# Kernel tuning notes

Hardware: AMD Instinct MI355X
Metric: run time of the kernel (lower is better)

The kernel has to match this reference:

```python
import jax, jax.numpy as jnp
import numpy as np

B, N, HIST, D, E, NH = 1024, 2, 64, 256, 128, 8
HD = D // NH


def _linear_params(key, fan_in, fan_out):
    kw, kb = jax.random.split(key)
    lim = 1.0 / np.sqrt(fan_in)
    W = jax.random.uniform(kw, (fan_in, fan_out), jnp.float32, -lim, lim)
    b = jax.random.uniform(kb, (fan_out,), jnp.float32, -lim, lim)
    return W, b


def setup_inputs() -> dict:
    key = jax.random.key(0)
    ks = jax.random.split(key, 11)
    inp = {
        "node_features": jax.random.normal(ks[0], (B, N, HIST, D), jnp.float32),
        "edge_features": jax.random.normal(ks[1], (B, E), jnp.float32),
    }
    inp["Wq"], inp["bq"] = _linear_params(ks[2], D, D)
    inp["Wk"], inp["bk"] = _linear_params(ks[3], D, D)
    inp["Wv"], inp["bv"] = _linear_params(ks[4], D, D)
    inp["Wo"], inp["bo"] = _linear_params(ks[5], D, D)
    inp["Wbias"], inp["bbias"] = _linear_params(ks[6], E, NH)
    inp["Wgate"], inp["bgate"] = _linear_params(ks[7], E, D)
    inp["Wscale"], inp["bscale"] = _linear_params(ks[8], E, D)
    inp["Wshift"], inp["bshift"] = _linear_params(ks[9], E, D)
    inp["Whead"], inp["bhead"] = _linear_params(ks[10], E, NH)
    return inp


def reference(node_features, edge_features, Wq, bq, Wk, bk, Wv, bv, Wo, bo,
              Wbias, bbias, Wgate, bgate, Wscale, bscale, Wshift, bshift,
              Whead, bhead) -> jnp.ndarray:
    b, n, hist, d = node_features.shape
    s = n * hist  # seq_len (temporal mode)
    x = node_features.reshape(b, s, d)

    Q = x @ Wq + bq
    K = x @ Wk + bk
    V = x @ Wv + bv

    # Edge-conditioned modulation of V (ECC-style gate/scale/shift)
    gate = jax.nn.sigmoid(edge_features @ Wgate + bgate)      # [b, d]
    scale = jnp.tanh(edge_features @ Wscale + bscale)         # [b, d]
    shift = edge_features @ Wshift + bshift                   # [b, d]
    V = (V * (1.0 + scale[:, None, :]) + shift[:, None, :]) * gate[:, None, :]

    # [b, nh, s, hd]
    Q = Q.reshape(b, s, NH, HD).transpose(0, 2, 1, 3)
    K = K.reshape(b, s, NH, HD).transpose(0, 2, 1, 3)
    V = V.reshape(b, s, NH, HD).transpose(0, 2, 1, 3)

    scores = jnp.einsum('bhqd,bhkd->bhqk', Q, K) * (1.0 / np.sqrt(HD))

    edge_bias = edge_features @ Wbias + bbias                 # [b, nh]
    head_scale = jnp.tanh(edge_features @ Whead + bhead)      # [b, nh]
    scores = scores * (1.0 + head_scale[:, :, None, None])

    # attention bias: edge_bias placed at (t, hist+t) and (hist+t, t)
    t = jnp.arange(hist)
    eb = jnp.broadcast_to(edge_bias[:, :, None], (b, NH, hist))
    attention_bias = jnp.zeros((b, NH, s, s), scores.dtype)
    attention_bias = attention_bias.at[:, :, t, hist + t].set(eb)
    attention_bias = attention_bias.at[:, :, hist + t, t].set(eb)

    attn = jax.nn.softmax(scores + attention_bias, axis=-1)   # dropout in eval mode = identity
    out = jnp.einsum('bhqk,bhkd->bhqd', attn, V)
    out = out.transpose(0, 2, 1, 3).reshape(b, n, hist, d)
    out = out[:, :, -1, :]                                    # last timestep per node
    return out @ Wo + bo
```

## Files before the change

### kernel.cpp

```cpp
#include <hip/hip_runtime.h>
#include <cstdint>
#include <cstddef>


typedef short bf16x8 __attribute__((ext_vector_type(8)));
typedef float f32x4 __attribute__((ext_vector_type(4)));

#define MFMA16(A, B, C) __builtin_amdgcn_mfma_f32_16x16x32_bf16((A), (B), (C), 0, 0, 0)

static __device__ __forceinline__ uint16_t f2bf(float f) {
    uint32_t u = __builtin_bit_cast(uint32_t, f);
    u += 0x7FFFu + ((u >> 16) & 1u);
    return (uint16_t)(u >> 16);
}
static __device__ __forceinline__ uint32_t pack2(float a, float b) {
    return (uint32_t)f2bf(a) | ((uint32_t)f2bf(b) << 16);
}

__global__ __launch_bounds__(256) void k_prep(
    const float* __restrict__ Wq, const float* __restrict__ Wv,
    const float* __restrict__ Wo, const float* __restrict__ Wk,
    uint16_t* __restrict__ WqT, uint16_t* __restrict__ WvT,
    uint16_t* __restrict__ WoT, uint16_t* __restrict__ WkB,
    const float* __restrict__ edge,
    const float* __restrict__ Wgate, const float* __restrict__ bgate,
    const float* __restrict__ Wscale, const float* __restrict__ bscale,
    const float* __restrict__ Wshift, const float* __restrict__ bshift,
    const float* __restrict__ Wbias, const float* __restrict__ bbias,
    const float* __restrict__ Whead, const float* __restrict__ bhead,
    float* __restrict__ sp, float* __restrict__ tp, float* __restrict__ ebhs)
{
    __shared__ float smem[64 * 65];
    const int t = threadIdx.x;
    const int bid = blockIdx.x;
    if (bid < 64) {
        const int z = bid >> 4, tr = (bid >> 2) & 3, tc = bid & 3;
        if (z == 3) {
            #pragma unroll
            for (int i = 0; i < 16; i++) {
                int flat = i * 256 + t;
                int lr = flat >> 6, lc = flat & 63;
                WkB[(size_t)(tr * 64 + lr) * 264 + tc * 64 + lc] =
                    f2bf(Wk[(size_t)(tr * 64 + lr) * 256 + tc * 64 + lc]);
            }
            return;
        }
        const float* W = (z == 0) ? Wq : ((z == 1) ? Wv : Wo);
        uint16_t* O = (z == 0) ? WqT : ((z == 1) ? WvT : WoT);
        float (*tile)[65] = (float (*)[65])smem;
        #pragma unroll
        for (int i = 0; i < 16; i++) {
            int flat = i * 256 + t;
            int lr = flat >> 6, lc = flat & 63;
            tile[lr][lc] = W[(size_t)(tr * 64 + lr) * 256 + tc * 64 + lc];
        }
        __syncthreads();
        #pragma unroll
        for (int i = 0; i < 16; i++) {
            int flat = i * 256 + t;
            int orow = flat >> 6, oc = flat & 63;
            O[(size_t)(tc * 64 + orow) * 264 + tr * 64 + oc] = f2bf(tile[oc][orow]);
        }
        return;
    }
    float* eL = smem;
    const int b0 = (bid - 64) * 4;
    for (int idx = t; idx < 512; idx += 256) {
        int bi = idx >> 7, e = idx & 127;
        eL[bi * 128 + e] = edge[(size_t)(b0 + bi) * 128 + e];
    }
    __syncthreads();
    float ag[4] = {0, 0, 0, 0}, asr[4] = {0, 0, 0, 0}, ah[4] = {0, 0, 0, 0};
    for (int e = 0; e < 128; e++) {
        float wg = Wgate[e * 256 + t];
        float wsc = Wscale[e * 256 + t];
        float wsh = Wshift[e * 256 + t];
        #pragma unroll
        for (int bi = 0; bi < 4; bi++) {
            float xv = eL[bi * 128 + e];
            ag[bi] = fmaf(xv, wg, ag[bi]);
            asr[bi] = fmaf(xv, wsc, asr[bi]);
            ah[bi] = fmaf(xv, wsh, ah[bi]);
        }
    }
    float bg = bgate[t], bs = bscale[t], bsh = bshift[t];
    #pragma unroll
    for (int bi = 0; bi < 4; bi++) {
        float g = 1.0f / (1.0f + __expf(-(ag[bi] + bg)));
        float sc = tanhf(asr[bi] + bs);
        float sh = ah[bi] + bsh;
        sp[(size_t)(b0 + bi) * 256 + t] = (1.0f + sc) * g;
        tp[(size_t)(b0 + bi) * 256 + t] = sh * g;
    }
    if (t < 64) {
        int bi = t >> 4, o = t & 15, h = o & 7;
        const float* W = (o < 8) ? Wbias : Whead;
        float a = 0.0f;
        for (int e = 0; e < 128; e++) a = fmaf(eL[bi * 128 + e], W[e * 8 + h], a);
        float val = (o < 8) ? (a + bbias[h]) : tanhf(a + bhead[h]);
        ebhs[(size_t)(b0 + bi) * 16 + o] = val;
    }
}

__global__ __launch_bounds__(256) void k_qu(
    const float* __restrict__ node, const uint16_t* __restrict__ WqT,
    const uint16_t* __restrict__ WkB, const float* __restrict__ bq,
    uint16_t* __restrict__ U)
{
    __shared__ uint16_t xq[16 * 264];
    __shared__ uint16_t QL[16 * 264];
    const int t = threadIdx.x, lane = t & 63, w = t >> 6, c = lane & 15, quad = lane >> 4;
    const int b0 = blockIdx.x * 4;
    #pragma unroll
    for (int i = 0; i < 4; i++) {
        int flat4 = i * 256 + t;
        int row = flat4 >> 6, c4 = flat4 & 63;
        int r = row & 7;
        int bb = b0 + (r >> 1);
        int s = (r & 1) ? 127 : 63;
        const float4 v = *(const float4*)(node + ((size_t)(bb * 128 + s)) * 256 + c4 * 4);
        uint2 pv; pv.x = pack2(v.x, v.y); pv.y = pack2(v.z, v.w);
        *(uint2*)&xq[row * 264 + c4 * 4] = pv;
    }
    __syncthreads();
    f32x4 zero = {0, 0, 0, 0};
    f32x4 acc[4];
    #pragma unroll
    for (int i = 0; i < 4; i++) acc[i] = zero;
    #pragma unroll
    for (int kk = 0; kk < 8; kk++) {
        bf16x8 afr = *(const bf16x8*)&xq[c * 264 + kk * 32 + quad * 8];
        #pragma unroll
        for (int i = 0; i < 4; i++) {
            int nt = w * 4 + i;
            bf16x8 bfr = *(const bf16x8*)&WqT[(size_t)(nt * 16 + c) * 264 + kk * 32 + quad * 8];
            acc[i] = MFMA16(afr, bfr, acc[i]);
        }
    }
    #pragma unroll
    for (int i = 0; i < 4; i++) {
        int nt = w * 4 + i;
        float bqv = bq[nt * 16 + c];
        #pragma unroll
        for (int r = 0; r < 4; r++) {
            QL[(quad * 4 + r) * 264 + nt * 16 + c] = f2bf(acc[i][r] + bqv);
        }
    }
    __syncthreads();
    for (int hh = 0; hh < 8; hh++) {
        bf16x8 bfr = *(const bf16x8*)&QL[c * 264 + hh * 32 + quad * 8];
        #pragma unroll
        for (int i = 0; i < 4; i++) {
            int mt = w * 4 + i;
            bf16x8 afr = *(const bf16x8*)&WkB[(size_t)(mt * 16 + c) * 264 + hh * 32 + quad * 8];
            f32x4 d = MFMA16(afr, bfr, zero);
            if (c < 8) {
                int bb = b0 + (c >> 1);
                int qh = (c & 1) * 8 + hh;
                uint2 pk; pk.x = pack2(d[0], d[1]); pk.y = pack2(d[2], d[3]);
                *(uint2*)&U[((size_t)(bb * 16 + qh)) * 256 + mt * 16 + quad * 4] = pk;
            }
        }
    }
}

__global__ __launch_bounds__(256, 3) void k_main(
    const float* __restrict__ node,
    const uint16_t* __restrict__ U,
    const float* __restrict__ ebhs,
    uint16_t* __restrict__ Y)
{
    __shared__ uint16_t xc[64 * 264];
    __shared__ uint16_t uL[16 * 264];
    __shared__ uint16_t pL[16 * 72];
    __shared__ float wred[2][16][4];
    __shared__ float stM[16], stL[16], stA[16];
    __shared__ float ebhsL[16];
    const int b = blockIdx.x;
    const int t = threadIdx.x, lane = t & 63, w = t >> 6, c = lane & 15, quad = lane >> 4;
    #pragma unroll
    for (int i = 0; i < 2; i++) {
        int flat = i * 256 + t;
        int row = flat >> 5, c16 = flat & 31;
        uint4 v = *(const uint4*)&U[((size_t)b * 16 + row) * 256 + c16 * 8];
        *(uint4*)&uL[row * 264 + c16 * 8] = v;
    }
    if (t < 16) { ebhsL[t] = ebhs[(size_t)b * 16 + t]; stM[t] = -1e30f; stL[t] = 0.0f; }
    __syncthreads();
    const int q = c >> 3, h = c & 7;
    const float scaleF = 0.17677669529663687f * (1.0f + ebhsL[8 + h]);
    const float ebv = ebhsL[h];
    f32x4 zero = {0, 0, 0, 0};
    f32x4 yacc[4];
    #pragma unroll
    for (int tt = 0; tt < 4; tt++) yacc[tt] = zero;

    for (int ch = 0; ch < 2; ch++) {
        #pragma unroll
        for (int i = 0; i < 16; i++) {
            int flat4 = i * 256 + t;
            int row = flat4 >> 6, c4 = flat4 & 63;
            const float4 v = *(const float4*)(node + ((size_t)b * 128 + ch * 64 + row) * 256 + c4 * 4);
            uint2 pv; pv.x = pack2(v.x, v.y); pv.y = pack2(v.z, v.w);
            int col = (c4 * 4 + ((row >> 3) & 3) * 16) & 255;
            *(uint2*)&xc[row * 264 + col] = pv;
        }
        __syncthreads();
        f32x4 sacc = zero;
        {
            int arow = w * 16 + c;
            int sh = ((arow >> 3) & 3) * 16;
            #pragma unroll
            for (int kk = 0; kk < 8; kk++) {
                int colA = (kk * 32 + quad * 8 + sh) & 255;
                bf16x8 afr = *(const bf16x8*)&xc[arow * 264 + colA];
                bf16x8 bfr = *(const bf16x8*)&uL[c * 264 + kk * 32 + quad * 8];
                sacc = MFMA16(afr, bfr, sacc);
            }
        }
        float v0[4];
        #pragma unroll
        for (int r = 0; r < 4; r++) {
            int krow = ch * 64 + w * 16 + quad * 4 + r;
            float x = sacc[r] * scaleF;
            if ((q == 0 && krow == 127) || (q == 1 && krow == 63)) x += ebv;
            v0[r] = x;
        }
        float lmax = fmaxf(fmaxf(v0[0], v0[1]), fmaxf(v0[2], v0[3]));
        lmax = fmaxf(lmax, __shfl_xor(lmax, 16, 64));
        lmax = fmaxf(lmax, __shfl_xor(lmax, 32, 64));
        if (lane < 16) wred[0][c][w] = lmax;
        __syncthreads();
        float cmax = fmaxf(fmaxf(wred[0][c][0], wred[0][c][1]), fmaxf(wred[0][c][2], wred[0][c][3]));
        float mold = stM[c];
        float mnew = fmaxf(mold, cmax);
        float alpha = __expf(mold - mnew);
        float p0[4]; float lsum = 0.0f;
        #pragma unroll
        for (int r = 0; r < 4; r++) { p0[r] = __expf(v0[r] - mnew); lsum += p0[r]; }
        lsum += __shfl_xor(lsum, 16, 64);
        lsum += __shfl_xor(lsum, 32, 64);
        if (lane < 16) wred[1][c][w] = lsum;
        __syncthreads();
        if (w == 0 && lane < 16) {
            float csum = wred[1][c][0] + wred[1][c][1] + wred[1][c][2] + wred[1][c][3];
            stL[c] = stL[c] * alpha + csum;
            stM[c] = mnew;
            stA[c] = alpha;
        }
        {
            uint2 pk; pk.x = pack2(p0[0], p0[1]); pk.y = pack2(p0[2], p0[3]);
            *(uint2*)&pL[c * 72 + w * 16 + quad * 4] = pk;
        }
        __syncthreads();
        float av[4];
        #pragma unroll
        for (int r = 0; r < 4; r++) av[r] = stA[quad * 4 + r];
        #pragma unroll
        for (int tt = 0; tt < 4; tt++)
            #pragma unroll
            for (int r = 0; r < 4; r++) yacc[tt][r] *= av[r];
        #pragma unroll
        for (int kk = 0; kk < 2; kk++) {
            bf16x8 afr = *(const bf16x8*)&pL[c * 72 + kk * 32 + quad * 8];
            int kbase = kk * 32 + quad * 8;
            int sh = ((kbase >> 3) & 3) * 16;
            #pragma unroll
            for (int tt = 0; tt < 4; tt++) {
                int n = w * 64 + tt * 16 + c;
                int col = (n + sh) & 255;
                union { bf16x8 v; uint32_t u[4]; } bb;
                #pragma unroll
                for (int jj = 0; jj < 4; jj++) {
                    uint32_t lo = xc[(kbase + 2 * jj) * 264 + col];
                    uint32_t hi = xc[(kbase + 2 * jj + 1) * 264 + col];
                    bb.u[jj] = lo | (hi << 16);
                }
                yacc[tt] = MFMA16(afr, bb.v, yacc[tt]);
            }
        }
        __syncthreads();
    }
    float invl[4];
    #pragma unroll
    for (int r = 0; r < 4; r++) invl[r] = 1.0f / stL[quad * 4 + r];
    #pragma unroll
    for (int tt = 0; tt < 4; tt++) {
        int n = w * 64 + tt * 16 + c;
        #pragma unroll
        for (int r = 0; r < 4; r++) {
            int qh = quad * 4 + r;
            int hq = qh & 7, qq = qh >> 3;
            Y[((size_t)(hq * 2048 + b * 2 + qq)) * 256 + n] = f2bf(yacc[tt][r] * invl[r]);
        }
    }
}

__global__ __launch_bounds__(256) void k_out(
    const uint16_t* __restrict__ Y,
    const uint16_t* __restrict__ WvT, const uint16_t* __restrict__ WoT,
    const float* __restrict__ bv, const float* __restrict__ bo,
    const float* __restrict__ sp, const float* __restrict__ tp,
    float* __restrict__ out)
{
    __shared__ uint16_t yh[2 * 16 * 264];
    __shared__ uint16_t zm[16 * 264];
    const int t = threadIdx.x, lane = t & 63, w = t >> 6, c = lane & 15, quad = lane >> 4;
    const int R0 = blockIdx.x * 16;
    f32x4 zero = {0, 0, 0, 0};
    for (int hp = 0; hp < 4; hp++) {
        __syncthreads();
        #pragma unroll
        for (int i = 0; i < 4; i++) {
            int flat = i * 256 + t;
            int hl = flat >> 9, rem = flat & 511;
            int row = rem >> 5, c16 = rem & 31;
            uint4 v = *(const uint4*)&Y[((size_t)((2 * hp + hl) * 2048 + R0 + row)) * 256 + c16 * 8];
            *(uint4*)&yh[(hl * 16 + row) * 264 + c16 * 8] = v;
        }
        __syncthreads();
        int hl = w >> 1, nt = w & 1;
        int h = 2 * hp + hl;
        f32x4 zacc = zero;
        #pragma unroll
        for (int kk = 0; kk < 8; kk++) {
            bf16x8 afr = *(const bf16x8*)&yh[(hl * 16 + c) * 264 + kk * 32 + quad * 8];
            bf16x8 bfr = *(const bf16x8*)&WvT[(size_t)(h * 32 + nt * 16 + c) * 264 + kk * 32 + quad * 8];
            zacc = MFMA16(afr, bfr, zacc);
        }
        int col = h * 32 + nt * 16 + c;
        float bvv = bv[col];
        #pragma unroll
        for (int r = 0; r < 4; r++) {
            int row = quad * 4 + r;
            int b = (R0 + row) >> 1;
            float z = zacc[r] + bvv;
            zm[row * 264 + col] = f2bf(z * sp[(size_t)b * 256 + col] + tp[(size_t)b * 256 + col]);
        }
    }
    __syncthreads();
    #pragma unroll
    for (int i = 0; i < 4; i++) {
        int nt = w * 4 + i;
        int n = nt * 16 + c;
        f32x4 fa = zero;
        #pragma unroll
        for (int kk = 0; kk < 8; kk++) {
            bf16x8 afr = *(const bf16x8*)&zm[c * 264 + kk * 32 + quad * 8];
            bf16x8 bfr = *(const bf16x8*)&WoT[(size_t)n * 264 + kk * 32 + quad * 8];
            fa = MFMA16(afr, bfr, fa);
        }
        float bov = bo[n];
        #pragma unroll
        for (int r = 0; r < 4; r++) {
            out[(size_t)(R0 + quad * 4 + r) * 256 + n] = fa[r] + bov;
        }
    }
}

extern "C" void kernel_launch(void* const* d_in, const int* in_sizes, int n_in,
                              void* d_out, int out_size, void* d_ws, size_t ws_size,
                              hipStream_t stream) {
    const float* node   = (const float*)d_in[0];
    const float* edge   = (const float*)d_in[1];
    const float* Wq     = (const float*)d_in[2];
    const float* bq     = (const float*)d_in[3];
    const float* Wk     = (const float*)d_in[4];
    const float* Wv     = (const float*)d_in[6];
    const float* bv     = (const float*)d_in[7];
    const float* Wo     = (const float*)d_in[8];
    const float* bo     = (const float*)d_in[9];
    const float* Wbias  = (const float*)d_in[10];
    const float* bbias  = (const float*)d_in[11];
    const float* Wgate  = (const float*)d_in[12];
    const float* bgate  = (const float*)d_in[13];
    const float* Wscale = (const float*)d_in[14];
    const float* bscale = (const float*)d_in[15];
    const float* Wshift = (const float*)d_in[16];
    const float* bshift = (const float*)d_in[17];
    const float* Whead  = (const float*)d_in[18];
    const float* bhead  = (const float*)d_in[19];

    char* ws = (char*)d_ws;
    uint16_t* WqT  = (uint16_t*)(ws + 0);
    uint16_t* WvT  = (uint16_t*)(ws + 135168);
    uint16_t* WoT  = (uint16_t*)(ws + 270336);
    uint16_t* WkB  = (uint16_t*)(ws + 405504);
    float*    spw  = (float*)(ws + 540672);
    float*    tpw  = (float*)(ws + 1589248);
    float*    ebhs = (float*)(ws + 2637824);
    uint16_t* Uw   = (uint16_t*)(ws + 2703360);
    uint16_t* Yw   = (uint16_t*)(ws + 11091968);

    k_prep<<<320, 256, 0, stream>>>(Wq, Wv, Wo, Wk, WqT, WvT, WoT, WkB,
                                    edge, Wgate, bgate, Wscale, bscale, Wshift, bshift,
                                    Wbias, bbias, Whead, bhead, spw, tpw, ebhs);
    k_qu<<<256, 256, 0, stream>>>(node, WqT, WkB, bq, Uw);
    k_main<<<1024, 256, 0, stream>>>(node, Uw, ebhs, Yw);
    k_out<<<128, 256, 0, stream>>>(Yw, WvT, WoT, bv, bo, spw, tpw, (float*)d_out);
}
```

Baseline: 286.7 us.

## Compute full score rows per wave and prefetch second chunk into registers

```diff
diff --git a/kernel.cpp b/kernel.cpp
--- a/kernel.cpp
+++ b/kernel.cpp
@@ -172,12 +172,11 @@
 {
     __shared__ uint16_t xc[64 * 264];
     __shared__ uint16_t uL[16 * 264];
-    __shared__ uint16_t pL[16 * 72];
-    __shared__ float wred[2][16][4];
-    __shared__ float stM[16], stL[16], stA[16];
+    __shared__ uint16_t pL[4 * 16 * 72];
     __shared__ float ebhsL[16];
     const int b = blockIdx.x;
     const int t = threadIdx.x, lane = t & 63, w = t >> 6, c = lane & 15, quad = lane >> 4;
+
     #pragma unroll
     for (int i = 0; i < 2; i++) {
         int flat = i * 256 + t;
@@ -185,8 +184,25 @@
         uint4 v = *(const uint4*)&U[((size_t)b * 16 + row) * 256 + c16 * 8];
         *(uint4*)&uL[row * 264 + c16 * 8] = v;
     }
-    if (t < 16) { ebhsL[t] = ebhs[(size_t)b * 16 + t]; stM[t] = -1e30f; stL[t] = 0.0f; }
+    if (t < 16) ebhsL[t] = ebhs[(size_t)b * 16 + t];
+
+    float4 R[16];
+    #pragma unroll
+    for (int i = 0; i < 16; i++) {
+        int flat4 = i * 256 + t;
+        int row = flat4 >> 6, c4 = flat4 & 63;
+        R[i] = *(const float4*)(node + ((size_t)b * 128 + row) * 256 + c4 * 4);
+    }
+    #pragma unroll
+    for (int i = 0; i < 16; i++) {
+        int flat4 = i * 256 + t;
+        int row = flat4 >> 6, c4 = flat4 & 63;
+        uint2 pv; pv.x = pack2(R[i].x, R[i].y); pv.y = pack2(R[i].z, R[i].w);
+        int col = (c4 * 4 + ((row >> 3) & 3) * 16) & 255;
+        *(uint2*)&xc[row * 264 + col] = pv;
+    }
     __syncthreads();
+
     const int q = c >> 3, h = c & 7;
     const float scaleF = 0.17677669529663687f * (1.0f + ebhsL[8 + h]);
     const float ebv = ebhsL[h];
@@ -194,75 +210,76 @@
     f32x4 yacc[4];
     #pragma unroll
     for (int tt = 0; tt < 4; tt++) yacc[tt] = zero;
-
+    float mrow = -1e30f, lrow = 0.0f;
+    uint16_t* pW = &pL[w * 16 * 72];
+
+    #pragma unroll
     for (int ch = 0; ch < 2; ch++) {
-        #pragma unroll
-        for (int i = 0; i < 16; i++) {
-            int flat4 = i * 256 + t;
-            int row = flat4 >> 6, c4 = flat4 & 63;
-            const float4 v = *(const float4*)(node + ((size_t)b * 128 + ch * 64 + row) * 256 + c4 * 4);
-            uint2 pv; pv.x = pack2(v.x, v.y); pv.y = pack2(v.z, v.w);
-            int col = (c4 * 4 + ((row >> 3) & 3) * 16) & 255;
-            *(uint2*)&xc[row * 264 + col] = pv;
-        }
-        __syncthreads();
-        f32x4 sacc = zero;
-        {
-            int arow = w * 16 + c;
-            int sh = ((arow >> 3) & 3) * 16;
-            #pragma unroll
-            for (int kk = 0; kk < 8; kk++) {
+        if (ch == 0) {
+            #pragma unroll
+            for (int i = 0; i < 16; i++) {
+                int flat4 = i * 256 + t;
+                int row = flat4 >> 6, c4 = flat4 & 63;
+                R[i] = *(const float4*)(node + ((size_t)b * 128 + 64 + row) * 256 + c4 * 4);
+            }
+        }
+        f32x4 sacc[4];
+        #pragma unroll
+        for (int kt = 0; kt < 4; kt++) sacc[kt] = zero;
+        #pragma unroll
+        for (int kk = 0; kk < 8; kk++) {
+            bf16x8 bfr = *(const bf16x8*)&uL[c * 264 + kk * 32 + quad * 8];
+            #pragma unroll
+            for (int kt = 0; kt < 4; kt++) {
+                int arow = kt * 16 + c;
+                int sh = ((arow >> 3) & 3) * 16;
                 int colA = (kk * 32 + quad * 8 + sh) & 255;
                 bf16x8 afr = *(const bf16x8*)&xc[arow * 264 + colA];
-                bf16x8 bfr = *(const bf16x8*)&uL[c * 264 + kk * 32 + quad * 8];
-                sacc = MFMA16(afr, bfr, sacc);
-            }
-        }
-        float v0[4];
-        #pragma unroll
-        for (int r = 0; r < 4; r++) {
-            int krow = ch * 64 + w * 16 + quad * 4 + r;
-            float x = sacc[r] * scaleF;
-            if ((q == 0 && krow == 127) || (q == 1 && krow == 63)) x += ebv;
-            v0[r] = x;
-        }
-        float lmax = fmaxf(fmaxf(v0[0], v0[1]), fmaxf(v0[2], v0[3]));
+                sacc[kt] = MFMA16(afr, bfr, sacc[kt]);
+            }
+        }
+        float v0[4][4];
+        float lmax = -1e30f;
+        #pragma unroll
+        for (int kt = 0; kt < 4; kt++) {
+            #pragma unroll
+            for (int r = 0; r < 4; r++) {
+                int krow = ch * 64 + kt * 16 + quad * 4 + r;
+                float x = sacc[kt][r] * scaleF;
+                if ((q == 0 && krow == 127) || (q == 1 && krow == 63)) x += ebv;
+                v0[kt][r] = x;
+                lmax = fmaxf(lmax, x);
+            }
+        }
         lmax = fmaxf(lmax, __shfl_xor(lmax, 16, 64));
         lmax = fmaxf(lmax, __shfl_xor(lmax, 32, 64));
-        if (lane < 16) wred[0][c][w] = lmax;
-        __syncthreads();
-        float cmax = fmaxf(fmaxf(wred[0][c][0], wred[0][c][1]), fmaxf(wred[0][c][2], wred[0][c][3]));
-        float mold = stM[c];
-        float mnew = fmaxf(mold, cmax);
-        float alpha = __expf(mold - mnew);
-        float p0[4]; float lsum = 0.0f;
-        #pragma unroll
-        for (int r = 0; r < 4; r++) { p0[r] = __expf(v0[r] - mnew); lsum += p0[r]; }
+        float mnew = fmaxf(mrow, lmax);
+        float alpha = __expf(mrow - mnew);
+        float lsum = 0.0f;
+        #pragma unroll
+        for (int kt = 0; kt < 4; kt++) {
+            uint2 pk;
+            float p0 = __expf(v0[kt][0] - mnew);
+            float p1 = __expf(v0[kt][1] - mnew);
+            float p2 = __expf(v0[kt][2] - mnew);
+            float p3 = __expf(v0[kt][3] - mnew);
+            lsum += (p0 + p1) + (p2 + p3);
+            pk.x = pack2(p0, p1); pk.y = pack2(p2, p3);
+            *(uint2*)&pW[c * 72 + kt * 16 + quad * 4] = pk;
+        }
         lsum += __shfl_xor(lsum, 16, 64);
         lsum += __shfl_xor(lsum, 32, 64);
-        if (lane < 16) wred[1][c][w] = lsum;
-        __syncthreads();
-        if (w == 0 && lane < 16) {
-            float csum = wred[1][c][0] + wred[1][c][1] + wred[1][c][2] + wred[1][c][3];
-            stL[c] = stL[c] * alpha + csum;
-            stM[c] = mnew;
-            stA[c] = alpha;
-        }
-        {
-            uint2 pk; pk.x = pack2(p0[0], p0[1]); pk.y = pack2(p0[2], p0[3]);
-            *(uint2*)&pL[c * 72 + w * 16 + quad * 4] = pk;
-        }
-        __syncthreads();
-        float av[4];
-        #pragma unroll
-        for (int r = 0; r < 4; r++) av[r] = stA[quad * 4 + r];
-        #pragma unroll
-        for (int tt = 0; tt < 4; tt++)
-            #pragma unroll
-            for (int r = 0; r < 4; r++) yacc[tt][r] *= av[r];
+        lrow = lrow * alpha + lsum;
+        mrow = mnew;
+        #pragma unroll
+        for (int r = 0; r < 4; r++) {
+            float aj = __shfl(alpha, quad * 4 + r, 64);
+            #pragma unroll
+            for (int tt = 0; tt < 4; tt++) yacc[tt][r] *= aj;
+        }
         #pragma unroll
         for (int kk = 0; kk < 2; kk++) {
-            bf16x8 afr = *(const bf16x8*)&pL[c * 72 + kk * 32 + quad * 8];
+            bf16x8 afr = *(const bf16x8*)&pW[c * 72 + kk * 32 + quad * 8];
             int kbase = kk * 32 + quad * 8;
             int sh = ((kbase >> 3) & 3) * 16;
             #pragma unroll
@@ -279,19 +296,29 @@
                 yacc[tt] = MFMA16(afr, bb.v, yacc[tt]);
             }
         }
-        __syncthreads();
-    }
-    float invl[4];
-    #pragma unroll
-    for (int r = 0; r < 4; r++) invl[r] = 1.0f / stL[quad * 4 + r];
-    #pragma unroll
-    for (int tt = 0; tt < 4; tt++) {
-        int n = w * 64 + tt * 16 + c;
-        #pragma unroll
-        for (int r = 0; r < 4; r++) {
+        if (ch == 0) {
+            __syncthreads();
+            #pragma unroll
+            for (int i = 0; i < 16; i++) {
+                int flat4 = i * 256 + t;
+                int row = flat4 >> 6, c4 = flat4 & 63;
+                uint2 pv; pv.x = pack2(R[i].x, R[i].y); pv.y = pack2(R[i].z, R[i].w);
+                int col = (c4 * 4 + ((row >> 3) & 3) * 16) & 255;
+                *(uint2*)&xc[row * 264 + col] = pv;
+            }
+            __syncthreads();
+        }
+    }
+    float invr = 1.0f / lrow;
+    #pragma unroll
+    for (int r = 0; r < 4; r++) {
+        float invj = __shfl(invr, quad * 4 + r, 64);
+        #pragma unroll
+        for (int tt = 0; tt < 4; tt++) {
+            int n = w * 64 + tt * 16 + c;
             int qh = quad * 4 + r;
             int hq = qh & 7, qq = qh >> 3;
-            Y[((size_t)(hq * 2048 + b * 2 + qq)) * 256 + n] = f2bf(yacc[tt][r] * invl[r]);
+            Y[((size_t)(hq * 2048 + b * 2 + qq)) * 256 + n] = f2bf(yacc[tt][r] * invj);
         }
     }
 }
```

After: 290.0 us. No clear change (+1.2%).
